# Optimization experiments

Measured on AMD Instinct MI355X. Metric: run time of the kernel, lower is better.

## Reference

```python
import jax, jax.numpy as jnp
import numpy as np

B, S, D = 1, 2048, 4096
H, KVH, HD = 32, 8, 128
ROPE_THETA = 10000.0
RMS_EPS = 1e-5


def setup_inputs() -> dict:
    key = jax.random.key(0)
    k1, k2, k3 = jax.random.split(key, 3)
    scale = 1.0 / np.sqrt(D)
    return {
        "inputs_embeds": jax.random.normal(k1, (B, S, D), dtype=jnp.float32),
        "attention_mask": jnp.ones((B, S), dtype=jnp.float32),
        "g": jnp.ones((D,), dtype=jnp.float32),
        "Wq": jax.random.normal(k2, (D, H * HD), dtype=jnp.float32) * scale,
        "Wk": jax.random.normal(k3, (D, KVH * HD), dtype=jnp.float32) * scale,
    }


def _rotate_half(x):
    return jnp.concatenate([-x[..., HD // 2:], x[..., :HD // 2]], axis=-1)


def reference(inputs_embeds, attention_mask, g, Wq, Wk):
    # RMSNorm
    var = jnp.mean(jnp.square(inputs_embeds), axis=-1, keepdims=True)
    h = inputs_embeds * jax.lax.rsqrt(var + RMS_EPS) * g

    # QK projections -> [B, heads, S, HD]
    q = (h @ Wq).reshape(B, S, H, HD).transpose(0, 2, 1, 3)
    k = (h @ Wk).reshape(B, S, KVH, HD).transpose(0, 2, 1, 3)

    # RoPE (llama-style: cos/sin of duplicated half-dim freqs)
    pos = jnp.arange(S, dtype=jnp.float32)
    inv_freq = 1.0 / (ROPE_THETA ** (jnp.arange(0, HD, 2, dtype=jnp.float32) / HD))
    freqs = pos[:, None] * inv_freq[None, :]            # [S, HD/2]
    emb = jnp.concatenate([freqs, freqs], axis=-1)       # [S, HD]
    cos = jnp.cos(emb)[None, None]                       # [1,1,S,HD]
    sin = jnp.sin(emb)[None, None]
    q = q * cos + _rotate_half(q) * sin
    k = k * cos + _rotate_half(k) * sin

    # repeat_kv: expand KV heads to H query heads (grouped-query)
    k = jnp.repeat(k, H // KVH, axis=1)                  # [B,H,S,HD]

    # raw QK^T scores (no softmax/V)
    scores = jnp.einsum('bhqd,bhkd->bhqk', q, k) / np.float32(np.sqrt(HD))

    # causal mask + 2D padding mask (all-ones here -> pure causal)
    min_f = jnp.finfo(scores.dtype).min
    i = jnp.arange(S)[:, None]
    j = jnp.arange(S)[None, :]
    causal = jnp.where(j > i, min_f, jnp.float32(0.0))   # [S,S]
    pad = (causal[None, None] == 0.0) & (attention_mask[:, None, None, :] == 0.0)
    mask = jnp.where(pad, min_f, causal[None, None])     # [B,1,S,S]
    return scores + mask
```

## Files before the change

kernel.cpp:

```cpp
#include <hip/hip_runtime.h>
#include <hip/hip_bf16.h>
#include <math.h>

#define S_LEN 2048
#define D_DIM 4096
#define NTOT 5120

typedef _Float16 f16x8 __attribute__((ext_vector_type(8)));
typedef float f32x4 __attribute__((ext_vector_type(4)));

#define MASKF (-3.3895313892515355e+38f)

#define QCH_BASE 134217728ull
#define KCH_BASE 201326592ull

__device__ __forceinline__ void async_ld16(const void* g, void* l) {
  __builtin_amdgcn_global_load_lds((const __attribute__((address_space(1))) void*)g,
                                   (__attribute__((address_space(3))) void*)l, 16, 0, 0);
}

__global__ __launch_bounds__(256) void prep(const float* __restrict__ x,
                                            const float* __restrict__ g,
                                            _Float16* __restrict__ h,
                                            float* __restrict__ ct, float* __restrict__ st) {
  int b = blockIdx.x;
  if (b >= 2048) {
    int i = (b - 2048) * 256 + threadIdx.x;
    int s = i >> 6, f = i & 63;
    float inv = (float)(1.0 / pow(10000.0, (double)(2 * f) / 128.0));
    float ang = (float)s * inv;
    ct[i] = (float)cos((double)ang);
    st[i] = (float)sin((double)ang);
    return;
  }
  int s = b;
  int t = threadIdx.x, w = t >> 6, l = t & 63;
  const f32x4* xr = (const f32x4*)(x + (size_t)s * D_DIM);
  const f32x4* gr = (const f32x4*)g;
  f32x4 v[4];
  float ss = 0.f;
#pragma unroll
  for (int i = 0; i < 4; ++i) {
    v[i] = xr[t + i * 256];
    ss += v[i][0] * v[i][0] + v[i][1] * v[i][1] + v[i][2] * v[i][2] + v[i][3] * v[i][3];
  }
#pragma unroll
  for (int off = 32; off; off >>= 1) ss += __shfl_down(ss, off);
  __shared__ float red[4];
  if (l == 0) red[w] = ss;
  __syncthreads();
  float tot = red[0] + red[1] + red[2] + red[3];
  float scale = rsqrtf(tot * (1.f / D_DIM) + 1e-5f);
  _Float16* hr = h + (size_t)s * D_DIM;
#pragma unroll
  for (int i = 0; i < 4; ++i) {
    f32x4 gg = gr[t + i * 256];
    _Float16 o[4];
    o[0] = (_Float16)(v[i][0] * scale * gg[0]);
    o[1] = (_Float16)(v[i][1] * scale * gg[1]);
    o[2] = (_Float16)(v[i][2] * scale * gg[2]);
    o[3] = (_Float16)(v[i][3] * scale * gg[3]);
    *(short4*)(hr + (size_t)(t + i * 256) * 4) = *(short4*)o;
  }
}

__global__ __launch_bounds__(256) void transpose_both(const float* __restrict__ Wq,
                                                      const float* __restrict__ Wk,
                                                      _Float16* __restrict__ wt) {
  __shared__ float tile[32][33];
  int b = blockIdx.x;
  const float* W;
  _Float16* Wt;
  int N, tn, td;
  if (b < 16384) {
    W = Wq; Wt = wt; N = 4096;
    tn = b & 127; td = b >> 7;
  } else {
    int b2 = b - 16384;
    W = Wk; Wt = wt + (size_t)4096 * D_DIM; N = 1024;
    tn = b2 & 31; td = b2 >> 5;
  }
  int c = threadIdx.x & 31, r0 = threadIdx.x >> 5;
  int d0 = td * 32, n0 = tn * 32;
#pragma unroll
  for (int i = 0; i < 4; ++i) {
    int r = r0 + i * 8;
    tile[r][c] = W[(size_t)(d0 + r) * N + n0 + c];
  }
  __syncthreads();
#pragma unroll
  for (int i = 0; i < 4; ++i) {
    int r = r0 + i * 8;
    Wt[(size_t)(n0 + r) * D_DIM + d0 + c] = (_Float16)tile[c][r];
  }
}

__global__ __launch_bounds__(256, 2) void gemm_rope(const _Float16* __restrict__ A,
                                                    const _Float16* __restrict__ Bt,
                                                    const float* __restrict__ ct,
                                                    const float* __restrict__ st,
                                                    char* __restrict__ base, int K) {
  __shared__ _Float16 lds[128 * 128];
  _Float16* As = lds;
  _Float16* Bs = lds + 128 * 64;
  const int bid = blockIdx.x;
  const int xcd = bid & 7, idx = bid >> 3;
  const int flat = xcd * 80 + idx;
  const int bx = flat >> 4;
  const int by = flat & 15;
  const int brow = by * 128;
  const size_t bcol = (size_t)bx * 128;
  const int tid = threadIdx.x, w = tid >> 6, l = tid & 63;
  const int wr = w * 32;
  f32x4 acc[2][8] = {};

  int st_o[4], st_r[4], st_src[4];
#pragma unroll
  for (int p = 0; p < 4; ++p) {
    int ob = (p * 4 + w) * 1024;
    int o = ob + l * 16;
    int r = o >> 7;
    int slot = (o >> 4) & 7;
    st_o[p] = ob; st_r[p] = r; st_src[p] = slot ^ (r & 7);
  }

  for (int k0 = 0; k0 < K; k0 += 64) {
#pragma unroll
    for (int p = 0; p < 4; ++p) {
      async_ld16(A + (size_t)(brow + st_r[p]) * K + (k0 + st_src[p] * 8), (char*)As + st_o[p]);
      async_ld16(Bt + (bcol + st_r[p]) * K + (k0 + st_src[p] * 8), (char*)Bs + st_o[p]);
    }
    asm volatile("s_waitcnt vmcnt(0)" ::: "memory");
    __syncthreads();
#pragma unroll
    for (int ks = 0; ks < 2; ++ks) {
      int kslot = ks * 4 + (l >> 4);
      f16x8 af[2], bf[8];
#pragma unroll
      for (int m = 0; m < 2; ++m) {
        int row = wr + m * 16 + (l & 15);
        af[m] = *(const f16x8*)((const char*)As + row * 128 + ((kslot ^ (row & 7)) << 4));
      }
#pragma unroll
      for (int n = 0; n < 8; ++n) {
        int row = n * 16 + (l & 15);
        bf[n] = *(const f16x8*)((const char*)Bs + row * 128 + ((kslot ^ (row & 7)) << 4));
      }
#pragma unroll
      for (int m = 0; m < 2; ++m)
#pragma unroll
        for (int n = 0; n < 8; ++n)
          acc[m][n] = __builtin_amdgcn_mfma_f32_16x16x32_f16(af[m], bf[n], acc[m][n], 0, 0, 0);
    }
    __syncthreads();
  }

#pragma unroll
  for (int m = 0; m < 2; ++m)
#pragma unroll
    for (int n = 0; n < 8; ++n) {
      int col = n * 16 + (l & 15);
      int f = col & 63;
#pragma unroll
      for (int j = 0; j < 4; ++j) {
        int row = wr + m * 16 + ((l >> 4) << 2) + j;
        int s = brow + row;
        float v = acc[m][n][j];
        float p = acc[m][n ^ 4][j];
        float o = v * ct[s * 64 + f] + ((col < 64) ? -p : p) * st[s * 64 + f];
        lds[row * 128 + (col ^ ((row & 7) << 3))] = (_Float16)o;
      }
    }
  __syncthreads();

  {
    int row = tid >> 1, hh = tid & 1;
    int s = brow + row;
    int sw = (row & 7) << 3;
    int h = bx;
    char* dst;
    if (h < 32) {
      int cc = 2 * s + (h >> 4);
      dst = base + QCH_BASE + (size_t)(cc >> 10) * 16777216ull +
            (size_t)(cc & 1023) * 8192ull + 4096ull + (size_t)((h & 15) * 128 + hh * 64) * 2;
    } else {
      int kv = h - 32;
      dst = base + KCH_BASE + (size_t)(s >> 1) * 8192ull + 4096ull +
            (size_t)(s & 1) * 2048ull + (size_t)(kv * 128 + hh * 64) * 2;
    }
#pragma unroll
    for (int k = 0; k < 8; ++k) {
      int c = hh * 64 + k * 8;
      f16x8 vv = *(const f16x8*)&lds[row * 128 + (c ^ sw)];
      *(f16x8*)(dst + k * 16) = vv;
    }
  }
}

__device__ __forceinline__ void fill_tile_f32(float* __restrict__ outh, int qi, int kj) {
  f32x4 mv = {MASKF, MASKF, MASKF, MASKF};
  int rr = threadIdx.x >> 5, cc = threadIdx.x & 31;
#pragma unroll
  for (int i = 0; i < 16; ++i) {
    int r = qi * 128 + i * 8 + rr;
    ((f32x4*)(outh + (size_t)r * S_LEN + kj * 128))[cc] = mv;
  }
}

__global__ __launch_bounds__(256, 2) void qk_full(const char* __restrict__ base,
                                                  const float* __restrict__ am,
                                                  float* __restrict__ out) {
  __shared__ _Float16 Qs[128 * 128], Ks[128 * 128];
  const int h = blockIdx.y;
  const int x = blockIdx.x;
  const int qi = (x & 7) + ((x >> 7) << 3);
  const int kj = (x >> 3) & 15;
  if (h >= 8 && h <= 12 && qi < 8 && kj >= 8) return;
  float* outh = out + (size_t)h * S_LEN * S_LEN;
  if (kj > qi) { fill_tile_f32(outh, qi, kj); return; }

  const int tid = threadIdx.x, w = tid >> 6, l = tid & 63;
  const int wr = (w >> 1) * 64, wc = (w & 1) * 64;
  const int hb = h >> 4;
  const size_t hoff = (size_t)(h & 15) * 256;
  const size_t kvoff = (size_t)(h >> 2) * 256;
#pragma unroll
  for (int p = 0; p < 8; ++p) {
    int ob = (p * 4 + w) * 1024;
    int o = ob + l * 16;
    int r = o >> 8;
    int slot = (o >> 4) & 15;
    int src = slot ^ (r & 7);
    int s = qi * 128 + r;
    int cc = 2 * s + hb;
    const char* qa = base + QCH_BASE + (size_t)(cc >> 10) * 16777216ull +
                     (size_t)(cc & 1023) * 8192ull + 4096ull + hoff + src * 16;
    int s2 = kj * 128 + r;
    const char* ka = base + KCH_BASE + (size_t)(s2 >> 1) * 8192ull + 4096ull +
                     (size_t)(s2 & 1) * 2048ull + kvoff + src * 16;
    async_ld16(qa, (char*)Qs + ob);
    async_ld16(ka, (char*)Ks + ob);
  }
  asm volatile("s_waitcnt vmcnt(0)" ::: "memory");
  __syncthreads();

  f32x4 acc[4][4] = {};
#pragma unroll
  for (int ks = 0; ks < 4; ++ks) {
    int kslot = ks * 4 + (l >> 4);
    f16x8 af[4], bf[4];
#pragma unroll
    for (int m = 0; m < 4; ++m) {
      int row = wr + m * 16 + (l & 15);
      af[m] = *(const f16x8*)((const char*)Qs + row * 256 + ((kslot ^ (row & 7)) << 4));
    }
#pragma unroll
    for (int n = 0; n < 4; ++n) {
      int row = wc + n * 16 + (l & 15);
      bf[n] = *(const f16x8*)((const char*)Ks + row * 256 + ((kslot ^ (row & 7)) << 4));
    }
#pragma unroll
    for (int m = 0; m < 4; ++m)
#pragma unroll
      for (int n = 0; n < 4; ++n)
        acc[m][n] = __builtin_amdgcn_mfma_f32_16x16x32_f16(af[m], bf[n], acc[m][n], 0, 0, 0);
  }

  const float sc = 0.088388347648318447f;
#pragma unroll
  for (int m = 0; m < 4; ++m) {
    int ib = qi * 128 + wr + m * 16 + ((l >> 4) << 2);
#pragma unroll
    for (int n = 0; n < 4; ++n) {
      int jg = kj * 128 + wc + n * 16 + (l & 15);
      float amv = am[jg];
#pragma unroll
      for (int j = 0; j < 4; ++j) {
        int i = ib + j;
        float v = acc[m][n][j] * sc;
        v = (v != v) ? 0.f : fminf(fmaxf(v, -3.38e38f), 3.38e38f);
        if (jg > i || amv == 0.f) v = MASKF;
        outh[(size_t)i * S_LEN + jg] = v;
      }
    }
  }
}

__global__ void fill_last(float* __restrict__ out) {
  int b = blockIdx.x;
  int h = 8 + (b >> 6);
  int t = b & 63;
  int qi = t >> 3, kj = 8 + (t & 7);
  fill_tile_f32(out + (size_t)h * S_LEN * S_LEN, qi, kj);
}

extern "C" void kernel_launch(void* const* d_in, const int* in_sizes, int n_in,
                              void* d_out, int out_size, void* d_ws, size_t ws_size,
                              hipStream_t stream) {
  const float* x  = (const float*)d_in[0];
  const float* am = (const float*)d_in[1];
  const float* g  = (const float*)d_in[2];
  const float* Wq = (const float*)d_in[3];
  const float* Wk = (const float*)d_in[4];
  float* out = (float*)d_out;
  char* ob = (char*)d_out;
  (void)d_ws; (void)ws_size;

  float*    ct   = (float*)(ob);
  float*    st   = (float*)(ob + 524288ull);
  _Float16* h16  = (_Float16*)(ob + 1048576ull);
  _Float16* wt   = (_Float16*)(ob + 17825792ull);

  prep<<<dim3(2560), dim3(256), 0, stream>>>(x, g, h16, ct, st);
  transpose_both<<<dim3(20480), dim3(256), 0, stream>>>(Wq, Wk, wt);
  gemm_rope<<<dim3(640), dim3(256), 0, stream>>>(h16, wt, ct, st, ob, 4096);
  qk_full<<<dim3(256, 32), dim3(256), 0, stream>>>(ob, am, out);
  fill_last<<<dim3(320), dim3(256), 0, stream>>>(out);
}
```

Measured before the change: 272.9 us.

## Load QK operands directly from global memory into registers, drop LDS staging

The qk_full kernel no longer stages Q and K tiles into shared memory through async global-to-LDS loads and a barrier. Each wave now reads its MFMA fragments straight from global memory, and the launch bound is raised to allow four blocks per CU, since no shared memory is allocated any more. This removes the LDS round trip and the sync, but each Q row is now loaded by two waves and each K row by two waves, so more traffic goes to L2. The global fragment loads are also 16-byte strided reads across rows rather than coalesced tile loads.

New measurement: 321.9 us. 1.18x slower.

```diff
diff --git a/kernel.cpp b/kernel.cpp
--- a/kernel.cpp
+++ b/kernel.cpp
@@ -207,10 +207,9 @@
   }
 }
 
-__global__ __launch_bounds__(256, 2) void qk_full(const char* __restrict__ base,
+__global__ __launch_bounds__(256, 4) void qk_full(const char* __restrict__ base,
                                                   const float* __restrict__ am,
                                                   float* __restrict__ out) {
-  __shared__ _Float16 Qs[128 * 128], Ks[128 * 128];
   const int h = blockIdx.y;
   const int x = blockIdx.x;
   const int qi = (x & 7) + ((x >> 7) << 3);
@@ -221,44 +220,33 @@
 
   const int tid = threadIdx.x, w = tid >> 6, l = tid & 63;
   const int wr = (w >> 1) * 64, wc = (w & 1) * 64;
+  const int ar = l & 15;
+  const int kg = l >> 4;
   const int hb = h >> 4;
   const size_t hoff = (size_t)(h & 15) * 256;
   const size_t kvoff = (size_t)(h >> 2) * 256;
-#pragma unroll
-  for (int p = 0; p < 8; ++p) {
-    int ob = (p * 4 + w) * 1024;
-    int o = ob + l * 16;
-    int r = o >> 8;
-    int slot = (o >> 4) & 15;
-    int src = slot ^ (r & 7);
-    int s = qi * 128 + r;
+
+  const char* qbase[4];
+  const char* kbase[4];
+#pragma unroll
+  for (int m = 0; m < 4; ++m) {
+    int s = qi * 128 + wr + m * 16 + ar;
     int cc = 2 * s + hb;
-    const char* qa = base + QCH_BASE + (size_t)(cc >> 10) * 16777216ull +
-                     (size_t)(cc & 1023) * 8192ull + 4096ull + hoff + src * 16;
-    int s2 = kj * 128 + r;
-    const char* ka = base + KCH_BASE + (size_t)(s2 >> 1) * 8192ull + 4096ull +
-                     (size_t)(s2 & 1) * 2048ull + kvoff + src * 16;
-    async_ld16(qa, (char*)Qs + ob);
-    async_ld16(ka, (char*)Ks + ob);
-  }
-  asm volatile("s_waitcnt vmcnt(0)" ::: "memory");
-  __syncthreads();
+    qbase[m] = base + QCH_BASE + (size_t)(cc >> 10) * 16777216ull +
+               (size_t)(cc & 1023) * 8192ull + 4096ull + hoff + kg * 16;
+    int s2 = kj * 128 + wc + m * 16 + ar;
+    kbase[m] = base + KCH_BASE + (size_t)(s2 >> 1) * 8192ull + 4096ull +
+               (size_t)(s2 & 1) * 2048ull + kvoff + kg * 16;
+  }
 
   f32x4 acc[4][4] = {};
 #pragma unroll
   for (int ks = 0; ks < 4; ++ks) {
-    int kslot = ks * 4 + (l >> 4);
     f16x8 af[4], bf[4];
 #pragma unroll
-    for (int m = 0; m < 4; ++m) {
-      int row = wr + m * 16 + (l & 15);
-      af[m] = *(const f16x8*)((const char*)Qs + row * 256 + ((kslot ^ (row & 7)) << 4));
-    }
-#pragma unroll
-    for (int n = 0; n < 4; ++n) {
-      int row = wc + n * 16 + (l & 15);
-      bf[n] = *(const f16x8*)((const char*)Ks + row * 256 + ((kslot ^ (row & 7)) << 4));
-    }
+    for (int m = 0; m < 4; ++m) af[m] = *(const f16x8*)(qbase[m] + ks * 64);
+#pragma unroll
+    for (int n = 0; n < 4; ++n) bf[n] = *(const f16x8*)(kbase[n] + ks * 64);
 #pragma unroll
     for (int m = 0; m < 4; ++m)
 #pragma unroll
```
